# Performance work log

Measured on AMD Instinct MI355X. Metric: run time of the kernel, lower is better.

Reference implementation:

```python
import jax, jax.numpy as jnp
import numpy as np
import math


def _rope(x, cos, sin):
    # x: [B, S, h, hd]; cos/sin: [S, hd//2]
    B, S, h, hd = x.shape
    xr = x.reshape(B, S, h, hd // 2, 2)
    x_re, x_im = xr[..., 0], xr[..., 1]
    c = cos[None, :, None, :]
    s = sin[None, :, None, :]
    out_re = x_re * c - x_im * s
    out_im = x_re * s + x_im * c
    return jnp.stack([out_re, out_im], axis=-1).reshape(B, S, h, hd)


def setup_inputs() -> dict:
    key = jax.random.key(0)
    ks = jax.random.split(key, 8)
    B, S, D = 2, 2048, 2048
    H, G = 16, 4
    hd = D // H  # 128
    q = jax.random.normal(ks[0], (B, S, D), dtype=jnp.float32)
    k = jax.random.normal(ks[1], (B, S, D), dtype=jnp.float32)
    v = jax.random.normal(ks[2], (B, S, D), dtype=jnp.float32)
    # causal mask, matching typical usage (mask==0 -> -inf)
    mask = jnp.broadcast_to(jnp.tril(jnp.ones((S, S), dtype=jnp.int32)), (B, S, S))
    # RoPE freqs: thetas = base**(-2*arange(0,hd,2)/hd), freq = outer(m, thetas)
    exp = -2.0 * jnp.arange(0, hd, 2, dtype=jnp.float32) / hd
    thetas = jnp.power(10000.0, exp)
    m = jnp.arange(S, dtype=jnp.float32)
    freq = jnp.outer(m, thetas)  # [S, hd//2]
    freq_cos = jnp.cos(freq)
    freq_sin = jnp.sin(freq)
    sc = 0.02
    W_q = jax.random.normal(ks[3], (D, D), dtype=jnp.float32) * sc
    W_k = jax.random.normal(ks[4], (D, D // G), dtype=jnp.float32) * sc
    W_v = jax.random.normal(ks[5], (D, D // G), dtype=jnp.float32) * sc
    W_o = jax.random.normal(ks[6], (D, D), dtype=jnp.float32) * sc
    return {"q": q, "k": k, "v": v, "mask": mask, "freq_cos": freq_cos,
            "freq_sin": freq_sin, "W_q": W_q, "W_k": W_k, "W_v": W_v,
            "W_o": W_o, "heads": 16, "group_size": 4}


def reference(q, k, v, mask, freq_cos, freq_sin, W_q, W_k, W_v, W_o, heads, group_size):
    B, S, D = q.shape
    H = heads
    Hkv = H // group_size
    hd = D // H
    qp = (q @ W_q).reshape(B, S, H, hd)
    kp = (k @ W_k).reshape(B, S, Hkv, hd)
    vp = (v @ W_v).reshape(B, S, Hkv, hd)
    qp = _rope(qp, freq_cos, freq_sin)
    kp = _rope(kp, freq_cos, freq_sin)
    # repeat_kv: each kv head repeated group_size times (group index inner)
    kp = jnp.repeat(kp, group_size, axis=2)  # [B,S,H,hd]
    vp = jnp.repeat(vp, group_size, axis=2)
    qh = qp.transpose(0, 2, 1, 3)  # [B,H,S,hd]
    kh = kp.transpose(0, 2, 1, 3)
    vh = vp.transpose(0, 2, 1, 3)
    scores = jnp.einsum('bhqd,bhkd->bhqk', qh, kh) / math.sqrt(hd)
    scores = jnp.where(mask[:, None, :, :] == 0, jnp.float32(-1e9), scores)
    attn = jax.nn.softmax(scores, axis=-1)
    out = jnp.einsum('bhqk,bhkd->bhqd', attn, vh)  # [B,H,S,hd]
    out = out.transpose(0, 2, 1, 3).reshape(B, S, D)
    return out @ W_o
```

## Files before the change

### kernel.cpp

```cpp
#include <hip/hip_runtime.h>

typedef __bf16 bf16;
typedef __attribute__((ext_vector_type(8))) __bf16 bf16x8;
typedef __attribute__((ext_vector_type(4))) __bf16 bf16x4;
typedef __attribute__((ext_vector_type(4))) float f32x4;

#define MFMA16(a, b, c) __builtin_amdgcn_mfma_f32_16x16x32_bf16((a), (b), (c), 0, 0, 0)

typedef __attribute__((address_space(1))) const void* gas_t;
typedef __attribute__((address_space(3))) void* las_t;
#define GLOAD_LDS16(g, l) \
    __builtin_amdgcn_global_load_lds((gas_t)(g), (las_t)(l), 16, 0, 0)

__device__ __forceinline__ unsigned pack2(float a, float b) {
    unsigned short ua = __builtin_bit_cast(unsigned short, (bf16)a);
    unsigned short ub = __builtin_bit_cast(unsigned short, (bf16)b);
    return ((unsigned)ub << 16) | (unsigned)ua;
}

__global__ void transpose_cvt4(const float* __restrict__ Wq,
                               const float* __restrict__ Wo,
                               const float* __restrict__ Wk,
                               const float* __restrict__ Wv,
                               bf16* __restrict__ WqT, bf16* __restrict__ WoT,
                               bf16* __restrict__ WkT, bf16* __restrict__ WvT) {
    __shared__ bf16 tile[32][33];
    int z = blockIdx.z;
    const float* W = (z == 0) ? Wq : (z == 1) ? Wo : (z == 2) ? Wk : Wv;
    bf16* Wt = (z == 0) ? WqT : (z == 1) ? WoT : (z == 2) ? WkT : WvT;
    int N = (z < 2) ? 2048 : 512;
    const int K = 2048;
    int n0 = blockIdx.x * 32;
    if (n0 >= N) return;
    int k0 = blockIdx.y * 32;
    int tx = threadIdx.x, ty = threadIdx.y;
#pragma unroll
    for (int j = 0; j < 4; ++j)
        tile[ty + j * 8][tx] = (bf16)W[(size_t)(k0 + ty + j * 8) * N + n0 + tx];
    __syncthreads();
#pragma unroll
    for (int j = 0; j < 4; ++j)
        Wt[(size_t)(n0 + ty + j * 8) * K + k0 + tx] = tile[tx][ty + j * 8];
}

__global__ __launch_bounds__(256) void gemm_q(
    const float* __restrict__ A, const bf16* __restrict__ Bt,
    bf16* __restrict__ Qp, const float* __restrict__ cosb,
    const float* __restrict__ sinb, float qscale) {
    const int Kk = 2048, Nn = 2048;
    __shared__ bf16 As[128 * 64];
    __shared__ bf16 Bs[128 * 64];
    int tid = threadIdx.x;
    int lane = tid & 63, wid = tid >> 6;
    int lr = lane & 15, lg = lane >> 4;
    int m0 = blockIdx.y * 128, n0 = blockIdx.x * 128;
    int wr = wid >> 1, wc = wid & 1;

    int srow = lane >> 3;
    int scol = ((lane & 7) ^ srow) << 3;
    const bf16* Bbase = Bt + (size_t)(n0 + wid * 32 + srow) * Kk + scol;

    int fragAr = wr * 64 + lr;
    int fragBr = wc * 64 + lr;
    int swz = lr & 7;

    f32x4 acc[4][4] = {};

    for (int kt = 0; kt < 32; ++kt) {
        int k0 = kt << 6;
#pragma unroll
        for (int i = 0; i < 8; ++i) {
            int slot = tid + i * 256;
            int row = slot >> 4, c4 = (slot & 15) << 2;
            f32x4 v = *reinterpret_cast<const f32x4*>(
                A + (size_t)(m0 + row) * Kk + k0 + c4);
            bf16x4 h;
            h[0] = (bf16)v[0]; h[1] = (bf16)v[1];
            h[2] = (bf16)v[2]; h[3] = (bf16)v[3];
            int blk = (c4 >> 3) ^ (row & 7);
            *reinterpret_cast<bf16x4*>(&As[row * 64 + (blk << 3) + (c4 & 7)]) = h;
        }
#pragma unroll
        for (int i = 0; i < 4; ++i)
            GLOAD_LDS16(Bbase + (size_t)(i * 8) * Kk + k0,
                        &Bs[(wid * 4 + i) * 512]);
        __syncthreads();
#pragma unroll
        for (int kk = 0; kk < 2; ++kk) {
            int colOff = ((((kk << 2) | lg) ^ swz) << 3);
            bf16x8 af[4], bfr[4];
#pragma unroll
            for (int mi = 0; mi < 4; ++mi)
                af[mi] = *reinterpret_cast<const bf16x8*>(
                    &As[(fragAr + mi * 16) * 64 + colOff]);
#pragma unroll
            for (int ni = 0; ni < 4; ++ni)
                bfr[ni] = *reinterpret_cast<const bf16x8*>(
                    &Bs[(fragBr + ni * 16) * 64 + colOff]);
#pragma unroll
            for (int mi = 0; mi < 4; ++mi)
#pragma unroll
                for (int ni = 0; ni < 4; ++ni)
                    acc[mi][ni] = MFMA16(af[mi], bfr[ni], acc[mi][ni]);
        }
        __syncthreads();
    }

    int m_base = m0 + wr * 64, n_base = n0 + wc * 64;
#pragma unroll
    for (int mi = 0; mi < 4; ++mi) {
#pragma unroll
        for (int ni = 0; ni < 4; ++ni) {
            f32x4 v = acc[mi][ni];
            int gn = n_base + ni * 16 + lr;
            int d = gn & 127, p = d >> 1;
            bool ev = ((d & 1) == 0);
#pragma unroll
            for (int r = 0; r < 4; ++r) {
                int gm = m_base + mi * 16 + lg * 4 + r;
                int s = gm & 2047;
                float cc = cosb[s * 64 + p];
                float ss = sinb[s * 64 + p];
                float oth = __shfl_xor(v[r], 1);
                v[r] = (ev ? (v[r] * cc - oth * ss)
                           : (oth * ss + v[r] * cc)) * qscale;
            }
#pragma unroll
            for (int r = 0; r < 4; ++r)
                Qp[(size_t)(m_base + mi * 16 + lg * 4 + r) * Nn + gn] =
                    (bf16)v[r];
        }
    }
}

__global__ __launch_bounds__(256) void gemm_kv(
    const float* __restrict__ kin, const float* __restrict__ vin,
    const bf16* __restrict__ WkT, const bf16* __restrict__ WvT,
    bf16* __restrict__ Kt, bf16* __restrict__ Vt,
    const float* __restrict__ cosb, const float* __restrict__ sinb) {
    const int Kk = 2048;
    __shared__ bf16 As[128 * 64];
    __shared__ bf16 Bs[128 * 64];
    bool isK = (blockIdx.z == 0);
    const float* A = isK ? kin : vin;
    const bf16* Bt = isK ? WkT : WvT;

    int tid = threadIdx.x;
    int lane = tid & 63, wid = tid >> 6;
    int lr = lane & 15, lg = lane >> 4;
    int m0 = blockIdx.y * 128, n0 = blockIdx.x * 128;
    int wr = wid >> 1, wc = wid & 1;

    int srow = lane >> 3;
    int scol = ((lane & 7) ^ srow) << 3;
    const bf16* Bbase = Bt + (size_t)(n0 + wid * 32 + srow) * Kk + scol;

    int fragAr = wr * 64 + lr;
    int fragBr = wc * 64 + lr;
    int swz = lr & 7;

    f32x4 acc[4][4] = {};

    for (int kt = 0; kt < 32; ++kt) {
        int k0 = kt << 6;
#pragma unroll
        for (int i = 0; i < 8; ++i) {
            int slot = tid + i * 256;
            int row = slot >> 4, c4 = (slot & 15) << 2;
            f32x4 v = *reinterpret_cast<const f32x4*>(
                A + (size_t)(m0 + row) * Kk + k0 + c4);
            bf16x4 h;
            h[0] = (bf16)v[0]; h[1] = (bf16)v[1];
            h[2] = (bf16)v[2]; h[3] = (bf16)v[3];
            int blk = (c4 >> 3) ^ (row & 7);
            *reinterpret_cast<bf16x4*>(&As[row * 64 + (blk << 3) + (c4 & 7)]) = h;
        }
#pragma unroll
        for (int i = 0; i < 4; ++i)
            GLOAD_LDS16(Bbase + (size_t)(i * 8) * Kk + k0,
                        &Bs[(wid * 4 + i) * 512]);
        __syncthreads();
#pragma unroll
        for (int kk = 0; kk < 2; ++kk) {
            int colOff = ((((kk << 2) | lg) ^ swz) << 3);
            bf16x8 af[4], bfr[4];
#pragma unroll
            for (int mi = 0; mi < 4; ++mi)
                af[mi] = *reinterpret_cast<const bf16x8*>(
                    &As[(fragAr + mi * 16) * 64 + colOff]);
#pragma unroll
            for (int ni = 0; ni < 4; ++ni)
                bfr[ni] = *reinterpret_cast<const bf16x8*>(
                    &Bs[(fragBr + ni * 16) * 64 + colOff]);
#pragma unroll
            for (int mi = 0; mi < 4; ++mi)
#pragma unroll
                for (int ni = 0; ni < 4; ++ni)
                    acc[mi][ni] = MFMA16(af[mi], bfr[ni], acc[mi][ni]);
        }
        __syncthreads();
    }

    int m_base = m0 + wr * 64, n_base = n0 + wc * 64;
#pragma unroll
    for (int mi = 0; mi < 4; ++mi) {
#pragma unroll
        for (int ni = 0; ni < 4; ++ni) {
            f32x4 v = acc[mi][ni];
            int gn = n_base + ni * 16 + lr;
            int hkv = gn >> 7, d = gn & 127;
            if (isK) {
                int p = d >> 1;
                bool ev = ((d & 1) == 0);
#pragma unroll
                for (int r = 0; r < 4; ++r) {
                    int gm = m_base + mi * 16 + lg * 4 + r;
                    int s = gm & 2047;
                    float cc = cosb[s * 64 + p];
                    float ss = sinb[s * 64 + p];
                    float oth = __shfl_xor(v[r], 1);
                    float rv = ev ? (v[r] * cc - oth * ss) : (oth * ss + v[r] * cc);
                    int bb = gm >> 11;
                    Kt[((size_t)(bb * 4 + hkv) * 2048 + s) * 128 + d] = (bf16)rv;
                }
            } else {
                int gm0 = m_base + mi * 16 + lg * 4;
                int bb = gm0 >> 11, s = gm0 & 2047;
                bf16x4 hh;
#pragma unroll
                for (int r = 0; r < 4; ++r) hh[r] = (bf16)v[r];
                *reinterpret_cast<bf16x4*>(
                    Vt + ((size_t)(bb * 4 + hkv) * 128 + d) * 2048 + s) = hh;
            }
        }
    }
}

__global__ __launch_bounds__(256) void gemm_o(
    const bf16* __restrict__ Ain, const bf16* __restrict__ Bt,
    float* __restrict__ Cout, int Nn, int Kk) {
    __shared__ bf16 As[128 * 64];
    __shared__ bf16 Bs[128 * 64];
    int tid = threadIdx.x;
    int lane = tid & 63, wid = tid >> 6;
    int lr = lane & 15, lg = lane >> 4;
    int m0 = blockIdx.y * 128, n0 = blockIdx.x * 128;
    int wr = wid >> 1, wc = wid & 1;

    int srow = lane >> 3;
    int scol = ((lane & 7) ^ srow) << 3;
    const bf16* Bbase = Bt + (size_t)(n0 + wid * 32 + srow) * Kk + scol;
    const bf16* Abase = Ain + (size_t)(m0 + wid * 32 + srow) * Kk + scol;

    int fragAr = wr * 64 + lr;
    int fragBr = wc * 64 + lr;
    int swz = lr & 7;

    f32x4 acc[4][4] = {};

    const int nk = Kk >> 6;
    for (int kt = 0; kt < nk; ++kt) {
        int k0 = kt << 6;
#pragma unroll
        for (int i = 0; i < 4; ++i) {
            GLOAD_LDS16(Abase + (size_t)(i * 8) * Kk + k0,
                        &As[(wid * 4 + i) * 512]);
            GLOAD_LDS16(Bbase + (size_t)(i * 8) * Kk + k0,
                        &Bs[(wid * 4 + i) * 512]);
        }
        __syncthreads();
#pragma unroll
        for (int kk = 0; kk < 2; ++kk) {
            int colOff = ((((kk << 2) | lg) ^ swz) << 3);
            bf16x8 af[4], bfr[4];
#pragma unroll
            for (int mi = 0; mi < 4; ++mi)
                af[mi] = *reinterpret_cast<const bf16x8*>(
                    &As[(fragAr + mi * 16) * 64 + colOff]);
#pragma unroll
            for (int ni = 0; ni < 4; ++ni)
                bfr[ni] = *reinterpret_cast<const bf16x8*>(
                    &Bs[(fragBr + ni * 16) * 64 + colOff]);
#pragma unroll
            for (int mi = 0; mi < 4; ++mi)
#pragma unroll
                for (int ni = 0; ni < 4; ++ni)
                    acc[mi][ni] = MFMA16(af[mi], bfr[ni], acc[mi][ni]);
        }
        __syncthreads();
    }

    int m_base = m0 + wr * 64, n_base = n0 + wc * 64;
#pragma unroll
    for (int mi = 0; mi < 4; ++mi)
#pragma unroll
        for (int ni = 0; ni < 4; ++ni) {
            f32x4 v = acc[mi][ni];
            int gn = n_base + ni * 16 + lr;
#pragma unroll
            for (int r = 0; r < 4; ++r)
                Cout[(size_t)(m_base + mi * 16 + lg * 4 + r) * Nn + gn] = v[r];
        }
}

__global__ __launch_bounds__(256) void attn_kernel(
    const bf16* __restrict__ Qp, const bf16* __restrict__ Kt,
    const bf16* __restrict__ Vt, bf16* __restrict__ Ao) {
    const int S = 2048, H = 16, HKV = 4, HD = 128;
    __shared__ bf16 Klds[64][136];
    __shared__ bf16 Vlds[128][72];

    int tid = threadIdx.x, lane = tid & 63, wid = tid >> 6;
    int lr = lane & 15, lg = lane >> 4;
    int h = blockIdx.x, b = blockIdx.y;
    int qt = (int)(gridDim.z - 1) - (int)blockIdx.z;
    int hkv = h >> 2;
    int q0 = qt * 64 + wid * 16;
    int qrow = q0 + lr;

    const bf16* Kbase = Kt + (size_t)(b * HKV + hkv) * S * HD;
    const bf16* Vbase = Vt + (size_t)(b * HKV + hkv) * HD * S;

    bf16x8 qf[4];
    {
        const bf16* qb = Qp + ((size_t)(b * S + qrow) * H + h) * HD;
#pragma unroll
        for (int ks = 0; ks < 4; ++ks)
            qf[ks] = *reinterpret_cast<const bf16x8*>(qb + ks * 32 + lg * 8);
    }

    f32x4 O[8] = {};
    float m_run = -3e38f, l_run = 0.f;
    int src0 = ((lane >> 4) & 1) * 32 + lr;
    int src1 = src0 + 16;
    bool h1 = (lg >> 1) != 0;

    int nkb = qt + 1;
    int k_r[4], k_c[4], v_r[4], v_c[4];
#pragma unroll
    for (int i = 0; i < 4; ++i) {
        int slot = tid + i * 256;
        k_r[i] = slot >> 4; k_c[i] = (slot & 15) << 3;
        v_r[i] = slot >> 3; v_c[i] = (slot & 7) << 3;
    }
    bf16x8 kreg[4], vreg[4];
#pragma unroll
    for (int i = 0; i < 4; ++i) {
        kreg[i] = *reinterpret_cast<const bf16x8*>(
            Kbase + (size_t)k_r[i] * HD + k_c[i]);
        vreg[i] = *reinterpret_cast<const bf16x8*>(
            Vbase + (size_t)v_r[i] * S + v_c[i]);
    }

    for (int kb = 0; kb < nkb; ++kb) {
        int s0 = kb * 64;
#pragma unroll
        for (int i = 0; i < 4; ++i) {
            *reinterpret_cast<bf16x8*>(&Klds[k_r[i]][k_c[i]]) = kreg[i];
            *reinterpret_cast<bf16x8*>(&Vlds[v_r[i]][v_c[i]]) = vreg[i];
        }
        __syncthreads();
        if (kb + 1 < nkb) {
            int sn = s0 + 64;
#pragma unroll
            for (int i = 0; i < 4; ++i) {
                kreg[i] = *reinterpret_cast<const bf16x8*>(
                    Kbase + (size_t)(sn + k_r[i]) * HD + k_c[i]);
                vreg[i] = *reinterpret_cast<const bf16x8*>(
                    Vbase + (size_t)v_r[i] * S + sn + v_c[i]);
            }
        }

        float p[4][4];
#pragma unroll
        for (int nt = 0; nt < 4; ++nt) {
            f32x4 sc = {};
#pragma unroll
            for (int ks = 0; ks < 4; ++ks) {
                bf16x8 kf = *reinterpret_cast<const bf16x8*>(
                    &Klds[nt * 16 + lr][ks * 32 + lg * 8]);
                sc = MFMA16(kf, qf[ks], sc);
            }
            if (kb == qt) {
                int sa = s0 + nt * 16 + lg * 4;
#pragma unroll
                for (int r = 0; r < 4; ++r)
                    p[nt][r] = (sa + r <= qrow) ? sc[r] : -1e30f;
            } else {
#pragma unroll
                for (int r = 0; r < 4; ++r) p[nt][r] = sc[r];
            }
        }
        float mx = p[0][0];
#pragma unroll
        for (int nt = 0; nt < 4; ++nt)
#pragma unroll
            for (int r = 0; r < 4; ++r) mx = fmaxf(mx, p[nt][r]);
        mx = fmaxf(mx, __shfl_xor(mx, 16));
        mx = fmaxf(mx, __shfl_xor(mx, 32));
        float mnew = fmaxf(m_run, mx);
        float al = exp2f(m_run - mnew);
        m_run = mnew;
        float rs = 0.f;
#pragma unroll
        for (int nt = 0; nt < 4; ++nt)
#pragma unroll
            for (int r = 0; r < 4; ++r) {
                p[nt][r] = exp2f(p[nt][r] - mnew);
                rs += p[nt][r];
            }
        rs += __shfl_xor(rs, 16);
        rs += __shfl_xor(rs, 32);
        l_run = l_run * al + rs;

        unsigned pk00 = pack2(p[0][0], p[0][1]), pk01 = pack2(p[0][2], p[0][3]);
        unsigned pk10 = pack2(p[1][0], p[1][1]), pk11 = pack2(p[1][2], p[1][3]);
        unsigned pk20 = pack2(p[2][0], p[2][1]), pk21 = pack2(p[2][2], p[2][3]);
        unsigned pk30 = pack2(p[3][0], p[3][1]), pk31 = pack2(p[3][2], p[3][3]);
        unsigned e00 = __shfl(pk00, src0), e01 = __shfl(pk01, src0);
        unsigned e10 = __shfl(pk10, src0), e11 = __shfl(pk11, src0);
        unsigned e20 = __shfl(pk20, src0), e21 = __shfl(pk21, src0);
        unsigned e30 = __shfl(pk30, src0), e31 = __shfl(pk31, src0);
        unsigned o00 = __shfl(pk00, src1), o01 = __shfl(pk01, src1);
        unsigned o10 = __shfl(pk10, src1), o11 = __shfl(pk11, src1);
        unsigned o20 = __shfl(pk20, src1), o21 = __shfl(pk21, src1);
        unsigned o30 = __shfl(pk30, src1), o31 = __shfl(pk31, src1);
        union U { unsigned u[4]; bf16x8 v; } P0, P1;
        P0.u[0] = h1 ? e10 : e00;
        P0.u[1] = h1 ? e11 : e01;
        P0.u[2] = h1 ? o10 : o00;
        P0.u[3] = h1 ? o11 : o01;
        P1.u[0] = h1 ? e30 : e20;
        P1.u[1] = h1 ? e31 : e21;
        P1.u[2] = h1 ? o30 : o20;
        P1.u[3] = h1 ? o31 : o21;

#pragma unroll
        for (int d2 = 0; d2 < 8; ++d2)
#pragma unroll
            for (int r = 0; r < 4; ++r) O[d2][r] *= al;
#pragma unroll
        for (int d2 = 0; d2 < 8; ++d2) {
            bf16x8 vf0 =
                *reinterpret_cast<const bf16x8*>(&Vlds[d2 * 16 + lr][lg * 8]);
            bf16x8 vf1 = *reinterpret_cast<const bf16x8*>(
                &Vlds[d2 * 16 + lr][32 + lg * 8]);
            O[d2] = MFMA16(vf0, P0.v, O[d2]);
            O[d2] = MFMA16(vf1, P1.v, O[d2]);
        }
        __syncthreads();
    }

    float inv = 1.0f / l_run;
    const size_t obase = ((size_t)(b * S + qrow) * H + h) * HD;
#pragma unroll
    for (int d2 = 0; d2 < 8; ++d2) {
        bf16x4 st;
#pragma unroll
        for (int r = 0; r < 4; ++r) st[r] = (bf16)(O[d2][r] * inv);
        *reinterpret_cast<bf16x4*>(const_cast<bf16*>(Ao) + obase + d2 * 16 +
                                   lg * 4) = st;
    }
}

extern "C" void kernel_launch(void* const* d_in, const int* in_sizes, int n_in,
                              void* d_out, int out_size, void* d_ws,
                              size_t ws_size, hipStream_t stream) {
    const float* q = (const float*)d_in[0];
    const float* k = (const float*)d_in[1];
    const float* v = (const float*)d_in[2];
    const float* fc = (const float*)d_in[4];
    const float* fs = (const float*)d_in[5];
    const float* Wq = (const float*)d_in[6];
    const float* Wk = (const float*)d_in[7];
    const float* Wv = (const float*)d_in[8];
    const float* Wo = (const float*)d_in[9];

    char* ws = (char*)d_ws;
    bf16* Wq_t = (bf16*)(ws + 0);
    bf16* Wk_t = (bf16*)(ws + 8388608);
    bf16* Wv_t = (bf16*)(ws + 10485760);
    bf16* Wo_t = (bf16*)(ws + 12582912);
    bf16* Qp   = (bf16*)(ws + 20971520);
    bf16* Kt   = (bf16*)(ws + 37748736);
    bf16* Vt   = (bf16*)(ws + 41943040);
    bf16* Ao   = (bf16*)(ws + 46137344);

    transpose_cvt4<<<dim3(64, 64, 4), dim3(32, 8), 0, stream>>>(
        Wq, Wo, Wk, Wv, Wq_t, Wo_t, Wk_t, Wv_t);

    const float qscale = 0.08838834764831845f * 1.4426950408889634f;

    gemm_q<<<dim3(16, 32), 256, 0, stream>>>(q, Wq_t, Qp, fc, fs, qscale);
    gemm_kv<<<dim3(4, 32, 2), 256, 0, stream>>>(k, v, Wk_t, Wv_t, Kt, Vt, fc,
                                                fs);

    attn_kernel<<<dim3(16, 2, 32), 256, 0, stream>>>(Qp, Kt, Vt, Ao);

    gemm_o<<<dim3(16, 32), 256, 0, stream>>>(Ao, Wo_t, (float*)d_out, 2048,
                                             2048);
}
```

Baseline: 270.4 us.

## Drop register prefetch of K/V tiles and raise wave priority around MFMA blocks

The flash-attention loop no longer prefetches the next K/V tile into registers during compute. Each iteration now loads its tile from global, stores it to LDS and synchronizes. s_setprio is raised around the QK^T and PV MFMA sections so those waves are favored by the scheduler. This frees registers, which may improve occupancy, but global load latency is now exposed unless other waves hide it.

```diff
diff --git a/kernel.cpp b/kernel.cpp
--- a/kernel.cpp
+++ b/kernel.cpp
@@ -335,43 +335,31 @@
     int src1 = src0 + 16;
     bool h1 = (lg >> 1) != 0;
 
-    int nkb = qt + 1;
-    int k_r[4], k_c[4], v_r[4], v_c[4];
-#pragma unroll
-    for (int i = 0; i < 4; ++i) {
-        int slot = tid + i * 256;
-        k_r[i] = slot >> 4; k_c[i] = (slot & 15) << 3;
-        v_r[i] = slot >> 3; v_c[i] = (slot & 7) << 3;
-    }
-    bf16x8 kreg[4], vreg[4];
-#pragma unroll
-    for (int i = 0; i < 4; ++i) {
-        kreg[i] = *reinterpret_cast<const bf16x8*>(
-            Kbase + (size_t)k_r[i] * HD + k_c[i]);
-        vreg[i] = *reinterpret_cast<const bf16x8*>(
-            Vbase + (size_t)v_r[i] * S + v_c[i]);
-    }
-
-    for (int kb = 0; kb < nkb; ++kb) {
+    for (int kb = 0; kb <= qt; ++kb) {
         int s0 = kb * 64;
+        bf16x8 kreg[4], vreg[4];
 #pragma unroll
         for (int i = 0; i < 4; ++i) {
-            *reinterpret_cast<bf16x8*>(&Klds[k_r[i]][k_c[i]]) = kreg[i];
-            *reinterpret_cast<bf16x8*>(&Vlds[v_r[i]][v_c[i]]) = vreg[i];
-        }
-        __syncthreads();
-        if (kb + 1 < nkb) {
-            int sn = s0 + 64;
-#pragma unroll
-            for (int i = 0; i < 4; ++i) {
-                kreg[i] = *reinterpret_cast<const bf16x8*>(
-                    Kbase + (size_t)(sn + k_r[i]) * HD + k_c[i]);
-                vreg[i] = *reinterpret_cast<const bf16x8*>(
-                    Vbase + (size_t)v_r[i] * S + sn + v_c[i]);
-            }
-        }
+            int slot = tid + i * 256;
+            int krow = slot >> 4, kc = (slot & 15) << 3;
+            kreg[i] = *reinterpret_cast<const bf16x8*>(
+                Kbase + (size_t)(s0 + krow) * HD + kc);
+            int vrow = slot >> 3, vc = (slot & 7) << 3;
+            vreg[i] = *reinterpret_cast<const bf16x8*>(
+                Vbase + (size_t)vrow * S + s0 + vc);
+        }
+#pragma unroll
+        for (int i = 0; i < 4; ++i) {
+            int slot = tid + i * 256;
+            int krow = slot >> 4, kc = (slot & 15) << 3;
+            *reinterpret_cast<bf16x8*>(&Klds[krow][kc]) = kreg[i];
+            int vrow = slot >> 3, vc = (slot & 7) << 3;
+            *reinterpret_cast<bf16x8*>(&Vlds[vrow][vc]) = vreg[i];
+        }
+        __syncthreads();
 
         float p[4][4];
+        __builtin_amdgcn_s_setprio(1);
 #pragma unroll
         for (int nt = 0; nt < 4; ++nt) {
             f32x4 sc = {};
@@ -391,6 +379,7 @@
                 for (int r = 0; r < 4; ++r) p[nt][r] = sc[r];
             }
         }
+        __builtin_amdgcn_s_setprio(0);
         float mx = p[0][0];
 #pragma unroll
         for (int nt = 0; nt < 4; ++nt)
@@ -439,6 +428,7 @@
         for (int d2 = 0; d2 < 8; ++d2)
 #pragma unroll
             for (int r = 0; r < 4; ++r) O[d2][r] *= al;
+        __builtin_amdgcn_s_setprio(1);
 #pragma unroll
         for (int d2 = 0; d2 < 8; ++d2) {
             bf16x8 vf0 =
@@ -448,6 +438,7 @@
             O[d2] = MFMA16(vf0, P0.v, O[d2]);
             O[d2] = MFMA16(vf1, P1.v, O[d2]);
         }
+        __builtin_amdgcn_s_setprio(0);
         __syncthreads();
     }
 
```

Measured after the change: 277.7 us. 1.03x slower.
